# Optimization experiments

Hardware: AMD Instinct MI355X
Metric: run time of the kernel (lower is better)

## Reference

```python
import jax, jax.numpy as jnp
import numpy as np

NUM_HEADS = 128
NUM_QK_BITS = 8
NUM_V_BITS = 8


def setup_inputs() -> dict:
    key = jax.random.key(0)
    ks = jax.random.split(key, 8)
    B, S, D = 2, 4096, 1024
    HQ = NUM_HEADS * NUM_QK_BITS  # 1024
    HV = NUM_HEADS * NUM_V_BITS   # 1024
    sc = 0.02
    return {
        "hidden_states": jax.random.normal(ks[0], (B, S, D), dtype=jnp.float32),
        "Wq": jax.random.normal(ks[1], (HQ, D), dtype=jnp.float32) * sc,
        "Wk": jax.random.normal(ks[2], (HQ, D), dtype=jnp.float32) * sc,
        "Wv": jax.random.normal(ks[3], (HV, D), dtype=jnp.float32) * sc,
        "Wo": jax.random.normal(ks[4], (D, HV), dtype=jnp.float32) * sc,
        "emb0": jax.random.normal(ks[5], (HV,), dtype=jnp.float32) * sc,
        "emb1": jax.random.normal(ks[6], (HV,), dtype=jnp.float32) * sc,
        "suffix_window": 8,
    }


def _rosa_forward(hidden_states, Wq, Wk, Wv, Wo, emb0, emb1, W):
    B, S, D = hidden_states.shape
    H, BQ, BV = NUM_HEADS, NUM_QK_BITS, NUM_V_BITS

    # projections -> [B, H, S, bits]
    q = (hidden_states @ Wq.T).reshape(B, S, H, BQ).transpose(0, 2, 1, 3)
    k = (hidden_states @ Wk.T).reshape(B, S, H, BQ).transpose(0, 2, 1, 3)
    v = (hidden_states @ Wv.T).reshape(B, S, H, BV).transpose(0, 2, 1, 3)

    # soft bits in [0, 1] (differentiable relaxation of bit quantization)
    qb = jax.nn.sigmoid(q)
    kb = jax.nn.sigmoid(k)
    vb = jax.nn.sigmoid(v)

    # causal suffix window: key/value at position t-d for offset d in [0, W)
    def shift(x, d):  # x: [B,H,S,C] -> x[t-d], front-padded with zeros
        return jnp.pad(x, ((0, 0), (0, 0), (d, 0), (0, 0)))[:, :, :S, :]

    kw = jnp.stack([shift(kb, d) for d in range(W)], axis=3)  # [B,H,S,W,BQ]
    vw = jnp.stack([shift(vb, d) for d in range(W)], axis=3)  # [B,H,S,W,BV]

    # Hamming-style agreement: sum_b [qb*kb + (1-qb)*(1-kb)]
    dot = jnp.einsum("bhsc,bhswc->bhsw", qb, kw)
    qsum = jnp.sum(qb, axis=-1)[..., None]        # [B,H,S,1]
    ksum = jnp.sum(kw, axis=-1)                   # [B,H,S,W]
    agree = BQ + 2.0 * dot - qsum - ksum          # [B,H,S,W]

    scale = 1.0 / jnp.sqrt(jnp.float32(BQ))
    scores = agree * scale

    # valid only when t - d >= 0
    valid = jnp.arange(S)[:, None] >= jnp.arange(W)[None, :]  # [S,W]
    scores = jnp.where(valid[None, None], scores, jnp.float32(-1e30))
    weights = jax.nn.softmax(scores, axis=-1)

    out = jnp.einsum("bhsw,bhswc->bhsc", weights, vw)  # [B,H,S,BV]
    out = out.transpose(0, 2, 1, 3).reshape(B, S, H * BV)

    # interpolation gate then output projection
    out = emb1 * out + emb0 * (1.0 - out)
    return out @ Wo.T


def reference(hidden_states, Wq, Wk, Wv, Wo, emb0, emb1, suffix_window):
    return _rosa_forward(hidden_states, Wq, Wk, Wv, Wo, emb0, emb1, suffix_window)
```

## Files before the change

kernel.cpp:

```cpp
#include <hip/hip_runtime.h>
#include <hip/hip_bf16.h>

typedef __bf16 bf16;
typedef __bf16 bf16x8 __attribute__((ext_vector_type(8)));
typedef int i32x4 __attribute__((ext_vector_type(4)));
typedef signed char scx8 __attribute__((ext_vector_type(8)));

__device__ __forceinline__ void gload_lds16(const void* g, void* l) {
  __builtin_amdgcn_global_load_lds(
      (const __attribute__((address_space(1))) void*)g,
      (__attribute__((address_space(3))) void*)l, 16, 0, 0);
}

template <int EPI>
__global__ __launch_bounds__(256, 3) void gemm_i8(
    const signed char* __restrict__ A, const signed char* __restrict__ Bw,
    const float* __restrict__ sA, const float* __restrict__ sB,
    const float* __restrict__ bias, void* __restrict__ C, int M, int N, int K) {
  __shared__ __align__(16) char smem[49152];
  const int tid = threadIdx.x;
  const int lane = tid & 63;
  const int wave = tid >> 6;

  const int nb = N >> 7;
  const int nwg = gridDim.x;
  const int q8 = nwg >> 3;
  const int tile = ((int)blockIdx.x & 7) * q8 + ((int)blockIdx.x >> 3);
  const int m0 = (tile / nb) << 7;
  const int n0 = (tile % nb) << 7;

  const int wm = (wave >> 1) << 6;
  const int wn = (wave & 1) << 6;

  i32x4 acc[4][4] = {};

  const int r_in = lane >> 2;
  const int swz = ((lane >> 3) & 3) << 4;
  const int scolb = ((lane & 3) << 4) ^ swz;
  const signed char* gA0 = A + (size_t)(m0 + (wave << 4) + r_in) * K + scolb;
  const signed char* gA1 = gA0 + ((size_t)K << 6);
  const signed char* gB0 = Bw + (size_t)(n0 + (wave << 4) + r_in) * K + scolb;
  const signed char* gB1 = gB0 + ((size_t)K << 6);
  const int ldsoff = (wave << 10) + (lane << 4);

  auto stage = [&](int buf) {
    char* b = smem + buf * 16384 + ldsoff;
    gload_lds16(gA0, b);
    gload_lds16(gA1, b + 4096);
    gload_lds16(gB0, b + 8192);
    gload_lds16(gB1, b + 12288);
    gA0 += 64; gA1 += 64; gB0 += 64; gB1 += 64;
  };

  const int lrow = lane & 15;
  const int koff = ((lane >> 4) << 4) ^ (((lrow >> 1) & 3) << 4);

  const int nt = K >> 6;

  stage(0);
  stage(1);

  int buf = 0, pb = 2;
  for (int t = 0; t < nt; ++t) {
    if (t == nt - 1) {
      asm volatile("s_waitcnt vmcnt(0)" ::: "memory");
    } else {
      asm volatile("s_waitcnt vmcnt(4)" ::: "memory");
    }
    __builtin_amdgcn_s_barrier();
    __builtin_amdgcn_sched_barrier(0);

    i32x4 af[4], bg[4];
    const char* base = smem + buf * 16384;
#pragma unroll
    for (int i = 0; i < 4; ++i) {
      af[i] = *(const i32x4*)(base + (wm + (i << 4) + lrow) * 64 + koff);
      bg[i] = *(const i32x4*)(base + 8192 + (wn + (i << 4) + lrow) * 64 + koff);
    }

    if (t + 2 < nt) stage(pb);

#pragma unroll
    for (int i = 0; i < 4; ++i)
#pragma unroll
      for (int j = 0; j < 4; ++j)
        acc[i][j] =
            __builtin_amdgcn_mfma_i32_16x16x64_i8(af[i], bg[j], acc[i][j], 0, 0, 0);

    if (++buf == 3) buf = 0;
    if (++pb == 3) pb = 0;
  }

  const int col0 = n0 + wn + lrow;
  const int rowb = m0 + wm + ((lane >> 4) << 2);
  float sb[4], bi[4];
#pragma unroll
  for (int j = 0; j < 4; ++j) {
    sb[j] = sB[col0 + (j << 4)];
    if (EPI == 0) bi[j] = bias[col0 + (j << 4)];
  }
#pragma unroll
  for (int i = 0; i < 4; ++i)
#pragma unroll
    for (int r = 0; r < 4; ++r) {
      const int row = rowb + (i << 4) + r;
      const float sa = (EPI == 1) ? sA[row] : (1.0f / 127.0f);
#pragma unroll
      for (int j = 0; j < 4; ++j) {
        const size_t idx = (size_t)row * N + (col0 + (j << 4));
        const float v = (float)acc[i][j][r] * (sa * sb[j]);
        if (EPI == 1) {
          ((bf16*)C)[idx] = (bf16)(1.0f / (1.0f + __expf(-v)));
        } else {
          ((float*)C)[idx] = v + bi[j];
        }
      }
    }
}

__global__ __launch_bounds__(256) void rosa_attn(
    const bf16* __restrict__ qkv, signed char* __restrict__ Oq) {
  const int t = blockIdx.x * 256 + threadIdx.x;
  const int row = t >> 7;
  const int h = t & 127;
  const int sp = row & 4095;

  const bf16* qptr = qkv + (size_t)row * 3072 + h * 8;
  bf16x8 qv = *(const bf16x8*)qptr;
  float qb[8], qsum = 0.f;
#pragma unroll
  for (int c = 0; c < 8; ++c) {
    qb[c] = (float)qv[c];
    qsum += qb[c];
  }

  float oacc[8] = {};
  float wsum = 0.f;
  const int wmax = (sp + 1 < 8) ? (sp + 1) : 8;
  const float scale = 0.35355339059327373f;

  for (int d = 0; d < wmax; ++d) {
    const bf16* base = qkv + (size_t)(row - d) * 3072 + h * 8;
    bf16x8 kv = *(const bf16x8*)(base + 1024);
    bf16x8 vv = *(const bf16x8*)(base + 2048);
    float dot = 0.f, ksum = 0.f;
#pragma unroll
    for (int c = 0; c < 8; ++c) {
      const float kb = (float)kv[c];
      dot += qb[c] * kb;
      ksum += kb;
    }
    const float score = (8.0f + 2.0f * dot - qsum - ksum) * scale;
    const float w = __expf(score);
    wsum += w;
#pragma unroll
    for (int c = 0; c < 8; ++c) oacc[c] += w * (float)vv[c];
  }

  const float inv = 127.0f / wsum;
  scx8 outv;
#pragma unroll
  for (int c = 0; c < 8; ++c)
    outv[c] = (signed char)(int)(oacc[c] * inv + 0.5f);
  *(scx8*)(Oq + (size_t)row * 1024 + h * 8) = outv;
}

__global__ __launch_bounds__(256) void quant_all(
    const float* __restrict__ X, const float* __restrict__ Wq,
    const float* __restrict__ Wk, const float* __restrict__ Wv,
    const float* __restrict__ Wo, const float* __restrict__ emb0,
    const float* __restrict__ emb1, signed char* __restrict__ Xq,
    signed char* __restrict__ Wqkvq, signed char* __restrict__ W2q,
    float* __restrict__ sx, float* __restrict__ sw, float* __restrict__ sw2,
    float* __restrict__ bias) {
  __shared__ float redm[4], reds[4];
  const int b = blockIdx.x, tid = threadIdx.x;
  const float* srow;
  signed char* drow;
  float* sc;
  bool isW2 = false;
  int w2r = 0;
  if (b < 8192) {
    srow = X + (size_t)b * 1024; drow = Xq + (size_t)b * 1024; sc = sx + b;
  } else if (b < 11264) {
    const int r = b - 8192;
    const float* w = (r < 1024) ? Wq : (r < 2048 ? Wk : Wv);
    srow = w + (size_t)(r & 1023) * 1024;
    drow = Wqkvq + (size_t)r * 1024; sc = sw + r;
  } else {
    const int r = b - 11264; w2r = r;
    srow = Wo + (size_t)r * 1024; drow = W2q + (size_t)r * 1024; sc = sw2 + r;
    isW2 = true;
  }
  float4 v = ((const float4*)srow)[tid];
  float bsum = 0.f;
  if (isW2) {
    const float4 e1 = ((const float4*)emb1)[tid];
    const float4 e0 = ((const float4*)emb0)[tid];
    bsum = v.x * e0.x + v.y * e0.y + v.z * e0.z + v.w * e0.w;
    v.x *= (e1.x - e0.x); v.y *= (e1.y - e0.y);
    v.z *= (e1.z - e0.z); v.w *= (e1.w - e0.w);
  }
  float m = fmaxf(fmaxf(fabsf(v.x), fabsf(v.y)), fmaxf(fabsf(v.z), fabsf(v.w)));
#pragma unroll
  for (int off = 32; off; off >>= 1) m = fmaxf(m, __shfl_xor(m, off));
#pragma unroll
  for (int off = 32; off; off >>= 1) bsum += __shfl_xor(bsum, off);
  if ((tid & 63) == 0) { redm[tid >> 6] = m; reds[tid >> 6] = bsum; }
  __syncthreads();
  const float mx = fmaxf(fmaxf(redm[0], redm[1]), fmaxf(redm[2], redm[3]));
  const float inv = (mx > 0.f) ? 127.f / mx : 0.f;
  const int q0 = __float2int_rn(v.x * inv) & 255;
  const int q1 = __float2int_rn(v.y * inv) & 255;
  const int q2 = __float2int_rn(v.z * inv) & 255;
  const int q3 = __float2int_rn(v.w * inv) & 255;
  ((int*)drow)[tid] = q0 | (q1 << 8) | (q2 << 16) | (q3 << 24);
  if (tid == 0) {
    *sc = (mx > 0.f) ? mx / 127.f : 0.f;
    if (isW2) bias[w2r] = reds[0] + reds[1] + reds[2] + reds[3];
  }
}

extern "C" void kernel_launch(void* const* d_in, const int* in_sizes, int n_in,
                              void* d_out, int out_size, void* d_ws,
                              size_t ws_size, hipStream_t stream) {
  const float* X = (const float*)d_in[0];
  const float* Wq = (const float*)d_in[1];
  const float* Wk = (const float*)d_in[2];
  const float* Wv = (const float*)d_in[3];
  const float* Wo = (const float*)d_in[4];
  const float* emb0 = (const float*)d_in[5];
  const float* emb1 = (const float*)d_in[6];

  char* ws = (char*)d_ws;
  signed char* Xq    = (signed char*)(ws + 0);
  signed char* Wqkvq = (signed char*)(ws + 8388608);
  signed char* W2q   = (signed char*)(ws + 11534336);
  float* sx   = (float*)(ws + 12582912);
  float* sw   = (float*)(ws + 12615680);
  float* sw2  = (float*)(ws + 12627968);
  float* bias = (float*)(ws + 12632064);
  bf16* QKVb  = (bf16*)(ws + 16777216);
  signed char* Oq = (signed char*)(ws + 67108864);
  float* out = (float*)d_out;

  quant_all<<<12288, 256, 0, stream>>>(X, Wq, Wk, Wv, Wo, emb0, emb1, Xq,
                                       Wqkvq, W2q, sx, sw, sw2, bias);

  gemm_i8<1><<<1536, 256, 0, stream>>>(Xq, Wqkvq, sx, sw, nullptr, QKVb, 8192,
                                       3072, 1024);

  rosa_attn<<<4096, 256, 0, stream>>>(QKVb, Oq);

  gemm_i8<0><<<512, 256, 0, stream>>>(Oq, W2q, nullptr, sw2, bias, out, 8192,
                                      1024, 1024);
}
```

Measured before the change: 99.80 us.

## Use smaller tiles in output GEMM and one wave per row in quantization

The output-projection GEMM gets its own kernel with 64x128 tiles, which doubles the grid from 512 to 1024 workgroups so the GPU's compute units are better filled. It also allows a smaller LDS footprint and higher occupancy. The quantization kernel now gives each wave one full row, with four float4 loads per lane, which removes the LDS reduction and block barrier. The trade-off is less data reuse per tile in the output GEMM and fewer threads in the quantization launch.

```diff
diff --git a/kernel.cpp b/kernel.cpp
--- a/kernel.cpp
+++ b/kernel.cpp
@@ -12,11 +12,10 @@
       (__attribute__((address_space(3))) void*)l, 16, 0, 0);
 }
 
-template <int EPI>
-__global__ __launch_bounds__(256, 3) void gemm_i8(
+__global__ __launch_bounds__(256, 3) void gemm_qkv(
     const signed char* __restrict__ A, const signed char* __restrict__ Bw,
     const float* __restrict__ sA, const float* __restrict__ sB,
-    const float* __restrict__ bias, void* __restrict__ C, int M, int N, int K) {
+    bf16* __restrict__ C, int M, int N, int K) {
   __shared__ __align__(16) char smem[49152];
   const int tid = threadIdx.x;
   const int lane = tid & 63;
@@ -93,27 +92,118 @@
 
   const int col0 = n0 + wn + lrow;
   const int rowb = m0 + wm + ((lane >> 4) << 2);
-  float sb[4], bi[4];
-#pragma unroll
-  for (int j = 0; j < 4; ++j) {
-    sb[j] = sB[col0 + (j << 4)];
-    if (EPI == 0) bi[j] = bias[col0 + (j << 4)];
-  }
+  float sb[4];
+#pragma unroll
+  for (int j = 0; j < 4; ++j) sb[j] = sB[col0 + (j << 4)];
 #pragma unroll
   for (int i = 0; i < 4; ++i)
 #pragma unroll
     for (int r = 0; r < 4; ++r) {
       const int row = rowb + (i << 4) + r;
-      const float sa = (EPI == 1) ? sA[row] : (1.0f / 127.0f);
+      const float sa = sA[row];
 #pragma unroll
       for (int j = 0; j < 4; ++j) {
         const size_t idx = (size_t)row * N + (col0 + (j << 4));
         const float v = (float)acc[i][j][r] * (sa * sb[j]);
-        if (EPI == 1) {
-          ((bf16*)C)[idx] = (bf16)(1.0f / (1.0f + __expf(-v)));
-        } else {
-          ((float*)C)[idx] = v + bi[j];
-        }
+        C[idx] = (bf16)(1.0f / (1.0f + __expf(-v)));
+      }
+    }
+}
+
+__global__ __launch_bounds__(256, 4) void gemm_out(
+    const signed char* __restrict__ A, const signed char* __restrict__ Bw,
+    const float* __restrict__ sB, const float* __restrict__ bias,
+    float* __restrict__ C, int M, int N, int K) {
+  __shared__ __align__(16) char smem[36864];
+  const int tid = threadIdx.x;
+  const int lane = tid & 63;
+  const int wave = tid >> 6;
+
+  const int nb = N >> 7;
+  const int nwg = gridDim.x;
+  const int q8 = nwg >> 3;
+  const int tile = ((int)blockIdx.x & 7) * q8 + ((int)blockIdx.x >> 3);
+  const int m0 = (tile / nb) << 6;
+  const int n0 = (tile % nb) << 7;
+
+  const int wm = (wave >> 1) << 5;
+  const int wn = (wave & 1) << 6;
+
+  i32x4 acc[2][4] = {};
+
+  const int r_in = lane >> 2;
+  const int swz = ((lane >> 3) & 3) << 4;
+  const int scolb = ((lane & 3) << 4) ^ swz;
+  const signed char* gA0 = A + (size_t)(m0 + (wave << 4) + r_in) * K + scolb;
+  const signed char* gB0 = Bw + (size_t)(n0 + (wave << 4) + r_in) * K + scolb;
+  const signed char* gB1 = gB0 + ((size_t)K << 6);
+  const int ldsoff = (wave << 10) + (lane << 4);
+
+  auto stage = [&](int buf) {
+    char* b = smem + buf * 12288 + ldsoff;
+    gload_lds16(gA0, b);
+    gload_lds16(gB0, b + 4096);
+    gload_lds16(gB1, b + 8192);
+    gA0 += 64; gB0 += 64; gB1 += 64;
+  };
+
+  const int lrow = lane & 15;
+  const int koff = ((lane >> 4) << 4) ^ (((lrow >> 1) & 3) << 4);
+
+  const int nt = K >> 6;
+
+  stage(0);
+  stage(1);
+
+  int buf = 0, pb = 2;
+  for (int t = 0; t < nt; ++t) {
+    if (t == nt - 1) {
+      asm volatile("s_waitcnt vmcnt(0)" ::: "memory");
+    } else {
+      asm volatile("s_waitcnt vmcnt(3)" ::: "memory");
+    }
+    __builtin_amdgcn_s_barrier();
+    __builtin_amdgcn_sched_barrier(0);
+
+    i32x4 af[2], bg[4];
+    const char* base = smem + buf * 12288;
+#pragma unroll
+    for (int i = 0; i < 2; ++i)
+      af[i] = *(const i32x4*)(base + (wm + (i << 4) + lrow) * 64 + koff);
+#pragma unroll
+    for (int j = 0; j < 4; ++j)
+      bg[j] = *(const i32x4*)(base + 4096 + (wn + (j << 4) + lrow) * 64 + koff);
+
+    if (t + 2 < nt) stage(pb);
+
+#pragma unroll
+    for (int i = 0; i < 2; ++i)
+#pragma unroll
+      for (int j = 0; j < 4; ++j)
+        acc[i][j] =
+            __builtin_amdgcn_mfma_i32_16x16x64_i8(af[i], bg[j], acc[i][j], 0, 0, 0);
+
+    if (++buf == 3) buf = 0;
+    if (++pb == 3) pb = 0;
+  }
+
+  const int col0 = n0 + wn + lrow;
+  const int rowb = m0 + wm + ((lane >> 4) << 2);
+  float sb[4], bi[4];
+#pragma unroll
+  for (int j = 0; j < 4; ++j) {
+    sb[j] = sB[col0 + (j << 4)] * (1.0f / 127.0f);
+    bi[j] = bias[col0 + (j << 4)];
+  }
+#pragma unroll
+  for (int i = 0; i < 2; ++i)
+#pragma unroll
+    for (int r = 0; r < 4; ++r) {
+      const int row = rowb + (i << 4) + r;
+#pragma unroll
+      for (int j = 0; j < 4; ++j) {
+        const size_t idx = (size_t)row * N + (col0 + (j << 4));
+        C[idx] = (float)acc[i][j][r] * sb[j] + bi[j];
       }
     }
 }
@@ -173,51 +263,59 @@
     signed char* __restrict__ Wqkvq, signed char* __restrict__ W2q,
     float* __restrict__ sx, float* __restrict__ sw, float* __restrict__ sw2,
     float* __restrict__ bias) {
-  __shared__ float redm[4], reds[4];
-  const int b = blockIdx.x, tid = threadIdx.x;
+  const int wrow = (blockIdx.x << 2) + ((threadIdx.x) >> 6);
+  const int lane = threadIdx.x & 63;
   const float* srow;
   signed char* drow;
   float* sc;
   bool isW2 = false;
   int w2r = 0;
-  if (b < 8192) {
-    srow = X + (size_t)b * 1024; drow = Xq + (size_t)b * 1024; sc = sx + b;
-  } else if (b < 11264) {
-    const int r = b - 8192;
+  if (wrow < 8192) {
+    srow = X + (size_t)wrow * 1024; drow = Xq + (size_t)wrow * 1024;
+    sc = sx + wrow;
+  } else if (wrow < 11264) {
+    const int r = wrow - 8192;
     const float* w = (r < 1024) ? Wq : (r < 2048 ? Wk : Wv);
     srow = w + (size_t)(r & 1023) * 1024;
     drow = Wqkvq + (size_t)r * 1024; sc = sw + r;
   } else {
-    const int r = b - 11264; w2r = r;
+    const int r = wrow - 11264; w2r = r;
     srow = Wo + (size_t)r * 1024; drow = W2q + (size_t)r * 1024; sc = sw2 + r;
     isW2 = true;
   }
-  float4 v = ((const float4*)srow)[tid];
-  float bsum = 0.f;
+  float4 v[4];
+  float bsum = 0.f, m = 0.f;
+#pragma unroll
+  for (int p = 0; p < 4; ++p) {
+    v[p] = ((const float4*)srow)[lane + (p << 6)];
+    if (isW2) {
+      const float4 e1 = ((const float4*)emb1)[lane + (p << 6)];
+      const float4 e0 = ((const float4*)emb0)[lane + (p << 6)];
+      bsum += v[p].x * e0.x + v[p].y * e0.y + v[p].z * e0.z + v[p].w * e0.w;
+      v[p].x *= (e1.x - e0.x); v[p].y *= (e1.y - e0.y);
+      v[p].z *= (e1.z - e0.z); v[p].w *= (e1.w - e0.w);
+    }
+    m = fmaxf(m, fmaxf(fmaxf(fabsf(v[p].x), fabsf(v[p].y)),
+                       fmaxf(fabsf(v[p].z), fabsf(v[p].w))));
+  }
+#pragma unroll
+  for (int off = 32; off; off >>= 1) m = fmaxf(m, __shfl_xor(m, off));
   if (isW2) {
-    const float4 e1 = ((const float4*)emb1)[tid];
-    const float4 e0 = ((const float4*)emb0)[tid];
-    bsum = v.x * e0.x + v.y * e0.y + v.z * e0.z + v.w * e0.w;
-    v.x *= (e1.x - e0.x); v.y *= (e1.y - e0.y);
-    v.z *= (e1.z - e0.z); v.w *= (e1.w - e0.w);
-  }
-  float m = fmaxf(fmaxf(fabsf(v.x), fabsf(v.y)), fmaxf(fabsf(v.z), fabsf(v.w)));
-#pragma unroll
-  for (int off = 32; off; off >>= 1) m = fmaxf(m, __shfl_xor(m, off));
-#pragma unroll
-  for (int off = 32; off; off >>= 1) bsum += __shfl_xor(bsum, off);
-  if ((tid & 63) == 0) { redm[tid >> 6] = m; reds[tid >> 6] = bsum; }
-  __syncthreads();
-  const float mx = fmaxf(fmaxf(redm[0], redm[1]), fmaxf(redm[2], redm[3]));
-  const float inv = (mx > 0.f) ? 127.f / mx : 0.f;
-  const int q0 = __float2int_rn(v.x * inv) & 255;
-  const int q1 = __float2int_rn(v.y * inv) & 255;
-  const int q2 = __float2int_rn(v.z * inv) & 255;
-  const int q3 = __float2int_rn(v.w * inv) & 255;
-  ((int*)drow)[tid] = q0 | (q1 << 8) | (q2 << 16) | (q3 << 24);
-  if (tid == 0) {
-    *sc = (mx > 0.f) ? mx / 127.f : 0.f;
-    if (isW2) bias[w2r] = reds[0] + reds[1] + reds[2] + reds[3];
+#pragma unroll
+    for (int off = 32; off; off >>= 1) bsum += __shfl_xor(bsum, off);
+  }
+  const float inv = (m > 0.f) ? 127.f / m : 0.f;
+#pragma unroll
+  for (int p = 0; p < 4; ++p) {
+    const int q0 = __float2int_rn(v[p].x * inv) & 255;
+    const int q1 = __float2int_rn(v[p].y * inv) & 255;
+    const int q2 = __float2int_rn(v[p].z * inv) & 255;
+    const int q3 = __float2int_rn(v[p].w * inv) & 255;
+    ((int*)drow)[lane + (p << 6)] = q0 | (q1 << 8) | (q2 << 16) | (q3 << 24);
+  }
+  if (lane == 0) {
+    *sc = (m > 0.f) ? m / 127.f : 0.f;
+    if (isW2) bias[w2r] = bsum;
   }
 }
 
@@ -244,14 +342,12 @@
   signed char* Oq = (signed char*)(ws + 67108864);
   float* out = (float*)d_out;
 
-  quant_all<<<12288, 256, 0, stream>>>(X, Wq, Wk, Wv, Wo, emb0, emb1, Xq,
-                                       Wqkvq, W2q, sx, sw, sw2, bias);
-
-  gemm_i8<1><<<1536, 256, 0, stream>>>(Xq, Wqkvq, sx, sw, nullptr, QKVb, 8192,
-                                       3072, 1024);
+  quant_all<<<3072, 256, 0, stream>>>(X, Wq, Wk, Wv, Wo, emb0, emb1, Xq,
+                                      Wqkvq, W2q, sx, sw, sw2, bias);
+
+  gemm_qkv<<<1536, 256, 0, stream>>>(Xq, Wqkvq, sx, sw, QKVb, 8192, 3072, 1024);
 
   rosa_attn<<<4096, 256, 0, stream>>>(QKVb, Oq);
 
-  gemm_i8<0><<<512, 256, 0, stream>>>(Oq, W2q, nullptr, sw2, bias, out, 8192,
-                                      1024, 1024);
-}
+  gemm_out<<<1024, 256, 0, stream>>>(Oq, W2q, sw2, bias, out, 8192, 1024, 1024);
+}
```

After: 98.85 us. Within noise of the previous version (-1.0%).
